# Kernel tuning notes

Hardware: AMD Instinct MI355X
Metric: run time of the kernel (lower is better)

## Reference

```python
import jax, jax.numpy as jnp
import numpy as np

N_NODES = 50000
N_EDGES = 1600000
NFEAT = 512
NHID = 64
H1 = 8      # nheads[0]
H2 = 1      # nheads[1]
NCLASS = 16
ALPHA = 0.2  # leaky_relu negative slope


def setup_inputs() -> dict:
    key = jax.random.key(0)
    ks = jax.random.split(key, 6)
    x = jax.random.normal(ks[0], (N_NODES, NFEAT), jnp.float32)
    edge_index = jax.random.randint(ks[1], (2, N_EDGES), 0, N_NODES, jnp.int32)

    def glorot(k, shape):
        fan_in, fan_out = shape[-2], shape[-1]
        std = (2.0 / (fan_in + fan_out)) ** 0.5
        return jax.random.normal(k, shape, jnp.float32) * std

    W1 = glorot(ks[2], (H1, NFEAT, NHID))
    a1 = jax.random.normal(ks[3], (H1, 2 * NHID), jnp.float32) * 0.1
    W2 = glorot(ks[4], (H2, NHID * H1, NCLASS))
    a2 = jax.random.normal(ks[5], (H2, 2 * NCLASS), jnp.float32) * 0.1
    return {"x": x, "edge_index": edge_index, "W1": W1, "a1": a1, "W2": W2, "a2": a2}


def _spgat_head(x, W, a, src, dst, n_nodes, apply_elu):
    # Sparse GAT head (pyGAT SpGraphAttentionLayer, eval mode / no dropout).
    h = x @ W                              # [N, F']
    f = W.shape[1]
    # a . [h_src || h_dst] decomposed into per-node scores (same math, no [E,2F'] concat)
    s_src = h @ a[:f]                      # [N]
    s_dst = h @ a[f:]                      # [N]
    logits = s_src[src] + s_dst[dst]       # [E]
    e = jnp.exp(-jax.nn.leaky_relu(logits, ALPHA))  # edge_e = exp(-leakyrelu(...)) > 0
    rowsum = jax.ops.segment_sum(e, src, num_segments=n_nodes)            # [N]
    agg = jax.ops.segment_sum(e[:, None] * h[dst], src, num_segments=n_nodes)  # [N, F']
    h_prime = agg / rowsum[:, None]
    return jax.nn.elu(h_prime) if apply_elu else h_prime


def reference(x, edge_index, W1, a1, W2, a2):
    src, dst = edge_index[0], edge_index[1]
    n = x.shape[0]
    # Layer 1: H1 heads, concat=True (elu inside each head), concatenated on features
    h = jnp.concatenate(
        [_spgat_head(x, W1[i], a1[i], src, dst, n, True) for i in range(W1.shape[0])],
        axis=1,
    )  # [N, H1*NHID]
    # Layer 2: H2 heads, concat=False, stacked then averaged
    outs = jnp.stack(
        [_spgat_head(h, W2[i], a2[i], src, dst, n, False) for i in range(W2.shape[0])],
        axis=2,
    )  # [N, NCLASS, H2]
    out = jnp.mean(outs, axis=2)
    return jax.nn.log_softmax(jax.nn.elu(out), axis=1)
```

## Files before the change

### kernel.cpp

```cpp
#include <hip/hip_runtime.h>

#define NN 50000
#define NE 1600000
#define NFEAT 512
#define NHID 64
#define H1 8
#define NCLASS 16
#define ALPHA 0.2f

#define BUCKETS 391
#define CAP 6144
#define EPB 4096
#define PASSA_BLKS 391
#define PASSB_BLKS 391
#define PACK_BLKS 1024
#define PACK2_BLKS 32
#define X8_BLKS 6250
#define GEMMB 391
#define NROW_PAD 50048

typedef __attribute__((ext_vector_type(8))) short short8;
typedef __attribute__((ext_vector_type(4))) float floatx4;
typedef __attribute__((ext_vector_type(2))) float floatx2;
typedef __attribute__((ext_vector_type(2))) long longx2;

__device__ __forceinline__ float elu_f(float x) { return x > 0.0f ? x : expf(x) - 1.0f; }
__device__ __forceinline__ float edge_w(float logit) {
    return expf(-fmaxf(logit, ALPHA * logit));
}
__device__ __forceinline__ ushort f2bf(float f) {
    uint u = __float_as_uint(f);
    return (ushort)((u + 0x7FFFu + ((u >> 16) & 1)) >> 16);
}
__device__ __forceinline__ uint packbf2(float lo, float hi) {
    return (uint)f2bf(lo) | ((uint)f2bf(hi) << 16);
}
__device__ __forceinline__ float bf2f(ushort v) { return __uint_as_float((uint)v << 16); }
__device__ __forceinline__ unsigned char f2fp8(float v) {
    return (unsigned char)(__builtin_amdgcn_cvt_pk_fp8_f32(v, v, 0, false) & 0xFF);
}
__device__ __forceinline__ uint pack4fp8(float a, float b, float c, float d) {
    uint u = __builtin_amdgcn_cvt_pk_fp8_f32(a, b, 0, false);
    return __builtin_amdgcn_cvt_pk_fp8_f32(c, d, u, true);
}

#define GLD16(g, l)                                                              \
    __builtin_amdgcn_global_load_lds(                                            \
        (const __attribute__((address_space(1))) unsigned int*)(g),              \
        (__attribute__((address_space(3))) unsigned int*)(l), 16, 0, 0)

__device__ __forceinline__ int scan256x(int v, int tid, int* wsum, int* tot) {
    int s = v;
#pragma unroll
    for (int o = 1; o < 64; o <<= 1) {
        int u = __shfl_up(s, o);
        if ((tid & 63) >= o) s += u;
    }
    __syncthreads();
    if ((tid & 63) == 63) wsum[tid >> 6] = s;
    __syncthreads();
    int off = 0, t = 0;
#pragma unroll
    for (int i = 0; i < 4; i++) {
        int x = wsum[i];
        if (i < (tid >> 6)) off += x;
        t += x;
    }
    *tot = t;
    return s - v + off;
}

__device__ __forceinline__ int scan512x(int v, int tid, int* wsum, int* tot) {
    int s = v;
#pragma unroll
    for (int o = 1; o < 64; o <<= 1) {
        int u = __shfl_up(s, o);
        if ((tid & 63) >= o) s += u;
    }
    __syncthreads();
    if ((tid & 63) == 63) wsum[tid >> 6] = s;
    __syncthreads();
    int off = 0, t = 0;
#pragma unroll
    for (int i = 0; i < 8; i++) {
        int x = wsum[i];
        if (i < (tid >> 6)) off += x;
        t += x;
    }
    *tot = t;
    return s - v + off;
}

__global__ __launch_bounds__(256) void prep_k(const float* __restrict__ W1,
                                              unsigned char* __restrict__ Wt8,
                                              const float* __restrict__ W2,
                                              ushort* __restrict__ W2tb,
                                              const float* __restrict__ x,
                                              unsigned char* x8,
                                              const int* __restrict__ ei,
                                              int* __restrict__ bucket_cnt,
                                              uint* __restrict__ staging) {
    int b = blockIdx.x;
    if (b < PACK_BLKS) {
        int i = b * 256 + threadIdx.x;
        int c = i >> 9, o = i & 511;
        int c6 = o >> 6, qhi = (o >> 4) & 3, kb = (o >> 3) & 1, bb = o & 7;
        int quad = qhi ^ ((c >> 1) & 3);
        int k = c6 * 64 + kb * 32 + quad * 8 + bb;
        Wt8[i] = f2fp8(W1[((c >> 6) * 512 + k) * 64 + (c & 63)]);
        return;
    }
    if (b < PACK_BLKS + PACK2_BLKS) {
        int i = (b - PACK_BLKS) * 256 + threadIdx.x;
        int c = i >> 9, f = i & 511;
        W2tb[i] = f2bf(W2[f * 16 + c]);
        return;
    }
    if (b < PACK_BLKS + PACK2_BLKS + X8_BLKS) {
        int i = (b - PACK_BLKS - PACK2_BLKS) * 256 + threadIdx.x;
        int row = i >> 5;
        int o0 = (i & 31) * 16;
        int c6 = o0 >> 6;
        int qhi = (o0 >> 4) & 3;
        int quad = qhi ^ ((row >> 1) & 3);
        const float* xp = x + (size_t)row * 512 + c6 * 64 + quad * 8;
        float4 v0 = *(const float4*)xp;
        float4 v1 = *(const float4*)(xp + 4);
        float4 v2 = *(const float4*)(xp + 32);
        float4 v3 = *(const float4*)(xp + 36);
        uint4 ov;
        ov.x = pack4fp8(v0.x, v0.y, v0.z, v0.w);
        ov.y = pack4fp8(v1.x, v1.y, v1.z, v1.w);
        ov.z = pack4fp8(v2.x, v2.y, v2.z, v2.w);
        ov.w = pack4fp8(v3.x, v3.y, v3.z, v3.w);
        *(uint4*)(x8 + (size_t)row * 512 + o0) = ov;
        return;
    }
    __shared__ int histA[BUCKETS];
    __shared__ int exclA[BUCKETS];
    __shared__ int baseA[BUCKETS];
    __shared__ int wsumA[4];
    __shared__ uint ebuf[EPB];
    const int blk = b - PACK_BLKS - PACK2_BLKS - X8_BLKS;
    const int t = threadIdx.x;
    const int e0 = blk * EPB;
    const int cntb = min(EPB, NE - e0);
    for (int i = t; i < BUCKETS; i += 256) histA[i] = 0;
    __syncthreads();
    int br[16]; uint pay[16];
#pragma unroll
    for (int i = 0; i < 16; i++) {
        int e = e0 + i * 256 + t;
        br[i] = -1;
        if (e < NE) {
            int s = ei[e], d = ei[NE + e];
            int bu = s >> 7;
            pay[i] = ((uint)bu << 23) | ((uint)(s & 127) << 16) | (uint)d;
            br[i] = (bu << 12) | atomicAdd(&histA[bu], 1);
        }
    }
    __syncthreads();
    int tot0, tot1;
    int v0 = histA[t];
    int v1 = (t + 256 < BUCKETS) ? histA[t + 256] : 0;
    int p0 = scan256x(v0, t, wsumA, &tot0);
    int p1 = scan256x(v1, t, wsumA, &tot1);
    exclA[t] = p0;
    if (t + 256 < BUCKETS) exclA[t + 256] = p1 + tot0;
    __syncthreads();
    for (int i = t; i < BUCKETS; i += 256) {
        int c = histA[i];
        if (c > 0) baseA[i] = atomicAdd(&bucket_cnt[i], c);
    }
#pragma unroll
    for (int i = 0; i < 16; i++)
        if (br[i] >= 0) ebuf[exclA[br[i] >> 12] + (br[i] & 4095)] = pay[i];
    __syncthreads();
    for (int j = t; j < cntb; j += 256) {
        uint v = ebuf[j];
        int bu = v >> 23;
        int pos = baseA[bu] + (j - exclA[bu]);
        staging[(size_t)bu * CAP + pos] = v;
    }
}

__global__ __launch_bounds__(64) void scan_k(const int* __restrict__ bucket_cnt,
                                             int* __restrict__ bucket_start,
                                             int* __restrict__ rowptr) {
    const int lane = threadIdx.x;
    int c[7]; int s0 = 0;
#pragma unroll
    for (int i = 0; i < 7; i++) {
        int b = lane * 7 + i;
        c[i] = (b < BUCKETS) ? bucket_cnt[b] : 0;
        s0 += c[i];
    }
    int sc = s0;
#pragma unroll
    for (int o = 1; o < 64; o <<= 1) {
        int u = __shfl_up(sc, o);
        if (lane >= o) sc += u;
    }
    int run = sc - s0;
#pragma unroll
    for (int i = 0; i < 7; i++) {
        int b = lane * 7 + i;
        if (b < BUCKETS) bucket_start[b] = run;
        run += c[i];
    }
    if (lane == 63) { bucket_start[BUCKETS] = run; rowptr[NN] = run; }
}

__global__ __launch_bounds__(512) void passb_gemm1_k(const int* __restrict__ bucket_cnt,
                                                     const int* __restrict__ bucket_start,
                                                     const uint* __restrict__ staging,
                                                     ushort* __restrict__ csru,
                                                     int* __restrict__ rowptr,
                                                     const unsigned char* __restrict__ Wt8,
                                                     const float* __restrict__ a1,
                                                     unsigned char* h8x8,
                                                     float* __restrict__ s1s,
                                                     float* __restrict__ s1d) {
    __shared__ unsigned char shmem[40960];
    const int tid = threadIdx.x;

    if (blockIdx.x < PASSB_BLKS) {
        int* hist2 = (int*)shmem;
        int* excl2 = hist2 + 128;
        int* cur2 = excl2 + 128;
        int* wsum2 = cur2 + 128;
        const int b = blockIdx.x;
        const int cnt = bucket_cnt[b];
        const int sbase = bucket_start[b];
        const uint* sg = staging + (size_t)b * CAP;
        if (tid < 128) { hist2[tid] = 0; cur2[tid] = 0; }
        __syncthreads();
        for (int e = tid; e < cnt; e += 512) atomicAdd(&hist2[(sg[e] >> 16) & 127], 1);
        __syncthreads();
        int v = (tid < 128) ? hist2[tid] : 0;
        int tot;
        int ex = scan512x(v, tid, wsum2, &tot);
        if (tid < 128) {
            excl2[tid] = ex;
            int n = b * 128 + tid;
            if (n < NN) rowptr[n] = sbase + ex;
        }
        __syncthreads();
        for (int e = tid; e < cnt; e += 512) {
            uint u = sg[e];
            int sl = (u >> 16) & 127;
            int pos = excl2[sl] + atomicAdd(&cur2[sl], 1);
            csru[sbase + pos] = (ushort)(u & 0xFFFF);
        }
        return;
    }

    unsigned char* As = shmem;
    unsigned char* Bs = shmem + 8192;
    const int gb = blockIdx.x - PASSB_BLKS;
    const int row0 = gb * 128;
    const int wv = tid >> 6, lane = tid & 63;
    const int l16 = lane & 15, quad = lane >> 4;
    const int qoff = ((quad ^ ((l16 >> 1) & 3)) << 4);
    const int mA = wv * 16 + (lane >> 2);
    const int offA = (lane & 3) * 16;
    const unsigned char* gA = h8x8 + (size_t)(row0 + mA) * 512 + offA;
    const unsigned char* gB0 = Wt8 + (size_t)(0 * 128 + mA) * 512 + offA;
    const unsigned char* gB1 = Wt8 + (size_t)(1 * 128 + mA) * 512 + offA;
    const unsigned char* gB2 = Wt8 + (size_t)(2 * 128 + mA) * 512 + offA;
    const unsigned char* gB3 = Wt8 + (size_t)(3 * 128 + mA) * 512 + offA;

    floatx4 acc[32];
#pragma unroll
    for (int ct = 0; ct < 32; ct++) acc[ct] = (floatx4){0.f, 0.f, 0.f, 0.f};

    for (int k0 = 0; k0 < 512; k0 += 64) {
        GLD16(gA + k0, As + wv * 1024);
        GLD16(gB0 + k0, Bs + wv * 1024);
        GLD16(gB1 + k0, Bs + 8192 + wv * 1024);
        GLD16(gB2 + k0, Bs + 16384 + wv * 1024);
        GLD16(gB3 + k0, Bs + 24576 + wv * 1024);
        __syncthreads();
        longx2 av = *(const longx2*)(As + (wv * 16 + l16) * 64 + qoff);
        const unsigned char* bp = Bs + l16 * 64 + qoff;
#pragma unroll
        for (int ct = 0; ct < 32; ct++) {
            longx2 bv = *(const longx2*)(bp + ct * 1024);
            acc[ct] = __builtin_amdgcn_mfma_f32_16x16x32_fp8_fp8(av.x, bv.x, acc[ct], 0, 0, 0);
            acc[ct] = __builtin_amdgcn_mfma_f32_16x16x32_fp8_fp8(av.y, bv.y, acc[ct], 0, 0, 0);
        }
        __syncthreads();
    }

    const int rbase = row0 + wv * 16 + quad * 4;
#pragma unroll
    for (int hh = 0; hh < 8; hh++) {
        float ss[4] = {0.f, 0.f, 0.f, 0.f}, sd[4] = {0.f, 0.f, 0.f, 0.f};
#pragma unroll
        for (int c4 = 0; c4 < 4; c4++) {
            int ct = hh * 4 + c4;
            int colg = ct * 16 + l16;
            float avs = a1[hh * 128 + c4 * 16 + l16];
            float avd = a1[hh * 128 + 64 + c4 * 16 + l16];
#pragma unroll
            for (int r = 0; r < 4; r++) {
                float v = acc[ct][r];
                ss[r] += v * avs;
                sd[r] += v * avd;
                int row = rbase + r;
                if (row < NN) h8x8[(size_t)row * 512 + colg] = f2fp8(v);
            }
        }
#pragma unroll
        for (int r = 0; r < 4; r++) {
            float a_ = ss[r], b_ = sd[r];
#pragma unroll
            for (int o = 1; o < 16; o <<= 1) {
                a_ += __shfl_xor(a_, o);
                b_ += __shfl_xor(b_, o);
            }
            int row = rbase + r;
            if (l16 == 0 && row < NN) {
                s1s[row * 8 + hh] = a_;
                s1d[row * 8 + hh] = b_;
            }
        }
    }
}

__global__ __launch_bounds__(256) void agg1f_k(const int* __restrict__ rowptr,
                                               const ushort* __restrict__ csru,
                                               const float* __restrict__ s1s,
                                               const float* __restrict__ s1d,
                                               const uint2* __restrict__ hb8,
                                               const ushort* __restrict__ W2tb,
                                               const float* __restrict__ a2,
                                               ushort* __restrict__ h2b,
                                               float* __restrict__ s2s,
                                               float* __restrict__ s2d) {
    __shared__ ushort Ash[16 * 512];
    const int tid = threadIdx.x;
    const int wv = tid >> 6, lane = tid & 63;
    const int n0 = blockIdx.x * 4;
    const int n = n0 + wv;
    const int head8 = lane >> 3;
    const int esub = lane & 7;
    const int beg = rowptr[n];
    const int deg = rowptr[n + 1] - beg;
    const float ssrc = s1s[n * 8 + head8];
    floatx2 acc[4] = {};
    float rsum = 0.f;

    int k = 0;
    for (; k + 8 <= deg; k += 8) {
        int dA = csru[beg + k + esub];
        float wA = edge_w(ssrc + s1d[dA * 8 + head8]);
        rsum += wA;
        int dj[8];
#pragma unroll
        for (int j = 0; j < 8; j++) dj[j] = __shfl(dA, j);
        uint2 v[8];
#pragma unroll
        for (int j = 0; j < 8; j++) v[j] = hb8[(uint)dj[j] * 64 + lane];
#pragma unroll
        for (int j = 0; j < 8; j++) {
            float wj = __shfl(wA, (head8 << 3) + j);
            floatx2 w2 = (floatx2){wj, wj};
            acc[0] += w2 * __builtin_amdgcn_cvt_pk_f32_fp8(v[j].x, false);
            acc[1] += w2 * __builtin_amdgcn_cvt_pk_f32_fp8(v[j].x, true);
            acc[2] += w2 * __builtin_amdgcn_cvt_pk_f32_fp8(v[j].y, false);
            acc[3] += w2 * __builtin_amdgcn_cvt_pk_f32_fp8(v[j].y, true);
        }
    }
    if (k < deg) {
        int jc = min(k + esub, deg - 1);
        int dwj = csru[beg + jc];
        float w = edge_w(ssrc + s1d[dwj * 8 + head8]);
        if (k + esub >= deg) w = 0.f;
        rsum += w;
        int rem = deg - k;
        for (int j = 0; j < rem; j++) {
            int djs = __shfl(dwj, j);
            uint2 vv = hb8[(uint)djs * 64 + lane];
            float wj = __shfl(w, (head8 << 3) + j);
            floatx2 w2 = (floatx2){wj, wj};
            acc[0] += w2 * __builtin_amdgcn_cvt_pk_f32_fp8(vv.x, false);
            acc[1] += w2 * __builtin_amdgcn_cvt_pk_f32_fp8(vv.x, true);
            acc[2] += w2 * __builtin_amdgcn_cvt_pk_f32_fp8(vv.y, false);
            acc[3] += w2 * __builtin_amdgcn_cvt_pk_f32_fp8(vv.y, true);
        }
    }

    rsum += __shfl_xor(rsum, 1);
    rsum += __shfl_xor(rsum, 2);
    rsum += __shfl_xor(rsum, 4);
    float inv = 1.0f / rsum;
    uint4 o;
    o.x = packbf2(elu_f(acc[0][0] * inv), elu_f(acc[0][1] * inv));
    o.y = packbf2(elu_f(acc[1][0] * inv), elu_f(acc[1][1] * inv));
    o.z = packbf2(elu_f(acc[2][0] * inv), elu_f(acc[2][1] * inv));
    o.w = packbf2(elu_f(acc[3][0] * inv), elu_f(acc[3][1] * inv));
    *(uint4*)(Ash + wv * 512 + lane * 8) = o;
    __syncthreads();

    if (wv == 0) {
        const int l16 = lane & 15, q = lane >> 4;
        floatx4 c2 = (floatx4){0.f, 0.f, 0.f, 0.f};
#pragma unroll
        for (int s = 0; s < 16; s++) {
            short8 af = *(const short8*)(Ash + l16 * 512 + s * 32 + q * 8);
            short8 bf = *(const short8*)(W2tb + l16 * 512 + s * 32 + q * 8);
            c2 = __builtin_amdgcn_mfma_f32_16x16x32_bf16(af, bf, c2, 0, 0, 0);
        }
        if (q == 0) {
#pragma unroll
            for (int r = 0; r < 4; r++) h2b[(size_t)(n0 + r) * 16 + l16] = f2bf(c2[r]);
        }
#pragma unroll
        for (int r = 0; r < 4; r++) {
            float ssv = c2[r] * a2[l16];
            float sdv = c2[r] * a2[16 + l16];
#pragma unroll
            for (int oo = 1; oo < 16; oo <<= 1) {
                ssv += __shfl_xor(ssv, oo);
                sdv += __shfl_xor(sdv, oo);
            }
            if (lane == 0) { s2s[n0 + r] = ssv; s2d[n0 + r] = sdv; }
        }
    }
}

__global__ __launch_bounds__(256) void agg2_k(const int* __restrict__ rowptr,
                                              const ushort* __restrict__ csru,
                                              const float* __restrict__ s2s,
                                              const float* __restrict__ s2d,
                                              const ushort* __restrict__ h2b,
                                              float* __restrict__ out) {
    const int n = (blockIdx.x * 256 + threadIdx.x) >> 6;
    const int lane = threadIdx.x & 63;
    if (n >= NN) return;
    const int beg = rowptr[n], end = rowptr[n + 1];
    const float sn = s2s[n];
    const int sub = lane >> 4, f = lane & 15;
    float acc = 0.f, rsum = 0.f;
    int e = beg + sub;
    for (; e + 12 < end; e += 16) {
        int d0 = csru[e], d1 = csru[e + 4], d2 = csru[e + 8], d3 = csru[e + 12];
        float t0 = s2d[d0], t1 = s2d[d1], t2 = s2d[d2], t3 = s2d[d3];
        float g0 = bf2f(h2b[(uint)d0 * 16 + f]), g1 = bf2f(h2b[(uint)d1 * 16 + f]);
        float g2 = bf2f(h2b[(uint)d2 * 16 + f]), g3 = bf2f(h2b[(uint)d3 * 16 + f]);
        float w0 = edge_w(sn + t0), w1 = edge_w(sn + t1);
        float w2 = edge_w(sn + t2), w3 = edge_w(sn + t3);
        acc += w0 * g0 + w1 * g1 + w2 * g2 + w3 * g3;
        rsum += w0 + w1 + w2 + w3;
    }
    for (; e < end; e += 4) {
        int d0 = csru[e];
        float w0 = edge_w(sn + s2d[d0]);
        acc += w0 * bf2f(h2b[(uint)d0 * 16 + f]);
        rsum += w0;
    }
    acc += __shfl_down(acc, 32);
    acc += __shfl_down(acc, 16);
    rsum += __shfl_down(rsum, 32);
    rsum += __shfl_down(rsum, 16);
    if (lane < 16) {
        float v = elu_f(acc / rsum);
        float m = v;
#pragma unroll
        for (int o = 8; o > 0; o >>= 1) m = fmaxf(m, __shfl_xor(m, o));
        float ex = expf(v - m), s = ex;
#pragma unroll
        for (int o = 8; o > 0; o >>= 1) s += __shfl_xor(s, o);
        out[(size_t)n * 16 + f] = v - (logf(s) + m);
    }
}

extern "C" void kernel_launch(void* const* d_in, const int* in_sizes, int n_in,
                              void* d_out, int out_size, void* d_ws, size_t ws_size,
                              hipStream_t stream) {
    const float* x  = (const float*)d_in[0];
    const int*   ei = (const int*)d_in[1];
    const float* W1 = (const float*)d_in[2];
    const float* a1 = (const float*)d_in[3];
    const float* W2 = (const float*)d_in[4];
    const float* a2 = (const float*)d_in[5];
    float* out = (float*)d_out;

    unsigned char* h8  = (unsigned char*)d_ws;
    unsigned char* Wt8 = h8 + (size_t)NROW_PAD * 512;
    ushort* W2tb  = (ushort*)(Wt8 + 512 * 512);
    float* s1s    = (float*)(W2tb + 8192);
    float* s1d    = s1s + (size_t)NN * H1;
    int* rowptr   = (int*)(s1d + (size_t)NN * H1);
    int* bucket_cnt   = rowptr + 50056;
    int* bucket_start = bucket_cnt + 512;
    ushort* csru  = (ushort*)(bucket_start + 512);
    ushort* h2b   = csru + NE;
    float* s2s    = (float*)(h2b + (size_t)NN * 16);
    float* s2d    = s2s + NN;
    uint* staging = (uint*)(s2d + NN);

    hipMemsetAsync(bucket_cnt, 0, 512 * sizeof(int), stream);

    prep_k<<<PACK_BLKS + PACK2_BLKS + X8_BLKS + PASSA_BLKS, 256, 0, stream>>>(
        W1, Wt8, W2, W2tb, x, h8, ei, bucket_cnt, staging);
    scan_k<<<1, 64, 0, stream>>>(bucket_cnt, bucket_start, rowptr);
    passb_gemm1_k<<<PASSB_BLKS + GEMMB, 512, 0, stream>>>(bucket_cnt, bucket_start,
                                                          staging, csru, rowptr,
                                                          Wt8, a1, h8, s1s, s1d);
    agg1f_k<<<NN / 4, 256, 0, stream>>>(rowptr, csru, s1s, s1d,
                                        (const uint2*)h8, W2tb, a2, h2b, s2s, s2d);
    agg2_k<<<(NN + 3) / 4, 256, 0, stream>>>(rowptr, csru, s2s, s2d, h2b, out);
}
```

Before: 401.4 us.

## Fold bucket scan into passB, prefetch edge scores, swizzle LDS, use fast exp

Removes the single-block scan kernel launch by having each passB block compute its own bucket offset with a wave-level prefix over the bucket counts. The layer-1 aggregation loop is restructured to merge the tail into the main loop and to prefetch the next group's neighbor indices and destination scores. The LDS staging buffer used by the MFMA is XOR-swizzled to reduce bank conflicts, and expf/logf calls become __expf/__logf. Each passB block now does the redundant scan work, and the fast intrinsics lower precision slightly.

```diff
diff --git a/kernel.cpp b/kernel.cpp
--- a/kernel.cpp
+++ b/kernel.cpp
@@ -24,9 +24,9 @@
 typedef __attribute__((ext_vector_type(2))) float floatx2;
 typedef __attribute__((ext_vector_type(2))) long longx2;
 
-__device__ __forceinline__ float elu_f(float x) { return x > 0.0f ? x : expf(x) - 1.0f; }
+__device__ __forceinline__ float elu_f(float x) { return x > 0.0f ? x : __expf(x) - 1.0f; }
 __device__ __forceinline__ float edge_w(float logit) {
-    return expf(-fmaxf(logit, ALPHA * logit));
+    return __expf(-fmaxf(logit, ALPHA * logit));
 }
 __device__ __forceinline__ ushort f2bf(float f) {
     uint u = __float_as_uint(f);
@@ -184,35 +184,7 @@
     }
 }
 
-__global__ __launch_bounds__(64) void scan_k(const int* __restrict__ bucket_cnt,
-                                             int* __restrict__ bucket_start,
-                                             int* __restrict__ rowptr) {
-    const int lane = threadIdx.x;
-    int c[7]; int s0 = 0;
-#pragma unroll
-    for (int i = 0; i < 7; i++) {
-        int b = lane * 7 + i;
-        c[i] = (b < BUCKETS) ? bucket_cnt[b] : 0;
-        s0 += c[i];
-    }
-    int sc = s0;
-#pragma unroll
-    for (int o = 1; o < 64; o <<= 1) {
-        int u = __shfl_up(sc, o);
-        if (lane >= o) sc += u;
-    }
-    int run = sc - s0;
-#pragma unroll
-    for (int i = 0; i < 7; i++) {
-        int b = lane * 7 + i;
-        if (b < BUCKETS) bucket_start[b] = run;
-        run += c[i];
-    }
-    if (lane == 63) { bucket_start[BUCKETS] = run; rowptr[NN] = run; }
-}
-
 __global__ __launch_bounds__(512) void passb_gemm1_k(const int* __restrict__ bucket_cnt,
-                                                     const int* __restrict__ bucket_start,
                                                      const uint* __restrict__ staging,
                                                      ushort* __restrict__ csru,
                                                      int* __restrict__ rowptr,
@@ -229,12 +201,35 @@
         int* excl2 = hist2 + 128;
         int* cur2 = excl2 + 128;
         int* wsum2 = cur2 + 128;
+        __shared__ int sbs;
         const int b = blockIdx.x;
         const int cnt = bucket_cnt[b];
-        const int sbase = bucket_start[b];
         const uint* sg = staging + (size_t)b * CAP;
         if (tid < 128) { hist2[tid] = 0; cur2[tid] = 0; }
+        if (tid < 64) {
+            int c[7]; int s0 = 0;
+#pragma unroll
+            for (int i = 0; i < 7; i++) {
+                int bi = tid * 7 + i;
+                c[i] = (bi < BUCKETS) ? bucket_cnt[bi] : 0;
+                s0 += c[i];
+            }
+            int sc = s0;
+#pragma unroll
+            for (int o = 1; o < 64; o <<= 1) {
+                int u = __shfl_up(sc, o);
+                if (tid >= o) sc += u;
+            }
+            int run = sc - s0;
+            if (tid == b / 7) {
+                int part = run;
+                for (int i = 0; i < b % 7; i++) part += c[i];
+                sbs = part;
+            }
+        }
+        if (b == 0 && tid == 0) rowptr[NN] = NE;
         __syncthreads();
+        const int sbase = sbs;
         for (int e = tid; e < cnt; e += 512) atomicAdd(&hist2[(sg[e] >> 16) & 127], 1);
         __syncthreads();
         int v = (tid < 128) ? hist2[tid] : 0;
@@ -339,11 +334,13 @@
                                                float* __restrict__ s2s,
                                                float* __restrict__ s2d) {
     __shared__ ushort Ash[16 * 512];
+    unsigned char* ashb = (unsigned char*)Ash;
     const int tid = threadIdx.x;
     const int wv = tid >> 6, lane = tid & 63;
     const int n0 = blockIdx.x * 4;
     const int n = n0 + wv;
     const int head8 = lane >> 3;
+    const int hb = head8 << 3;
     const int esub = lane & 7;
     const int beg = rowptr[n];
     const int deg = rowptr[n + 1] - beg;
@@ -351,43 +348,33 @@
     floatx2 acc[4] = {};
     float rsum = 0.f;
 
-    int k = 0;
-    for (; k + 8 <= deg; k += 8) {
-        int dA = csru[beg + k + esub];
-        float wA = edge_w(ssrc + s1d[dA * 8 + head8]);
-        rsum += wA;
-        int dj[8];
-#pragma unroll
-        for (int j = 0; j < 8; j++) dj[j] = __shfl(dA, j);
-        uint2 v[8];
-#pragma unroll
-        for (int j = 0; j < 8; j++) v[j] = hb8[(uint)dj[j] * 64 + lane];
-#pragma unroll
-        for (int j = 0; j < 8; j++) {
-            float wj = __shfl(wA, (head8 << 3) + j);
-            floatx2 w2 = (floatx2){wj, wj};
-            acc[0] += w2 * __builtin_amdgcn_cvt_pk_f32_fp8(v[j].x, false);
-            acc[1] += w2 * __builtin_amdgcn_cvt_pk_f32_fp8(v[j].x, true);
-            acc[2] += w2 * __builtin_amdgcn_cvt_pk_f32_fp8(v[j].y, false);
-            acc[3] += w2 * __builtin_amdgcn_cvt_pk_f32_fp8(v[j].y, true);
-        }
-    }
-    if (k < deg) {
-        int jc = min(k + esub, deg - 1);
-        int dwj = csru[beg + jc];
-        float w = edge_w(ssrc + s1d[dwj * 8 + head8]);
-        if (k + esub >= deg) w = 0.f;
-        rsum += w;
-        int rem = deg - k;
-        for (int j = 0; j < rem; j++) {
-            int djs = __shfl(dwj, j);
-            uint2 vv = hb8[(uint)djs * 64 + lane];
-            float wj = __shfl(w, (head8 << 3) + j);
-            floatx2 w2 = (floatx2){wj, wj};
-            acc[0] += w2 * __builtin_amdgcn_cvt_pk_f32_fp8(vv.x, false);
-            acc[1] += w2 * __builtin_amdgcn_cvt_pk_f32_fp8(vv.x, true);
-            acc[2] += w2 * __builtin_amdgcn_cvt_pk_f32_fp8(vv.y, false);
-            acc[3] += w2 * __builtin_amdgcn_cvt_pk_f32_fp8(vv.y, true);
+    const int G = (deg + 7) >> 3;
+    const int dm1 = deg - 1;
+    if (G > 0) {
+        int dA = csru[beg + min(esub, dm1)];
+        float tw = s1d[dA * 8 + head8];
+        for (int g = 0; g < G; g++) {
+            uint2 v[8];
+#pragma unroll
+            for (int j = 0; j < 8; j++) {
+                int dj = __shfl(dA, j);
+                v[j] = hb8[(uint)dj * 64 + lane];
+            }
+            int dAn = csru[beg + min(g * 8 + 8 + esub, dm1)];
+            float twn = s1d[dAn * 8 + head8];
+            float w = (g * 8 + esub <= dm1) ? edge_w(ssrc + tw) : 0.f;
+            rsum += w;
+#pragma unroll
+            for (int j = 0; j < 8; j++) {
+                float wj = __shfl(w, hb + j);
+                floatx2 w2 = (floatx2){wj, wj};
+                acc[0] += w2 * __builtin_amdgcn_cvt_pk_f32_fp8(v[j].x, false);
+                acc[1] += w2 * __builtin_amdgcn_cvt_pk_f32_fp8(v[j].x, true);
+                acc[2] += w2 * __builtin_amdgcn_cvt_pk_f32_fp8(v[j].y, false);
+                acc[3] += w2 * __builtin_amdgcn_cvt_pk_f32_fp8(v[j].y, true);
+            }
+            dA = dAn;
+            tw = twn;
         }
     }
 
@@ -400,7 +387,7 @@
     o.y = packbf2(elu_f(acc[1][0] * inv), elu_f(acc[1][1] * inv));
     o.z = packbf2(elu_f(acc[2][0] * inv), elu_f(acc[2][1] * inv));
     o.w = packbf2(elu_f(acc[3][0] * inv), elu_f(acc[3][1] * inv));
-    *(uint4*)(Ash + wv * 512 + lane * 8) = o;
+    *(uint4*)(ashb + wv * 1024 + ((lane * 16) ^ (wv << 4))) = o;
     __syncthreads();
 
     if (wv == 0) {
@@ -408,7 +395,8 @@
         floatx4 c2 = (floatx4){0.f, 0.f, 0.f, 0.f};
 #pragma unroll
         for (int s = 0; s < 16; s++) {
-            short8 af = *(const short8*)(Ash + l16 * 512 + s * 32 + q * 8);
+            short8 af = *(const short8*)(ashb + l16 * 1024 +
+                                         ((s * 64 + q * 16) ^ ((l16 & 7) << 4)));
             short8 bf = *(const short8*)(W2tb + l16 * 512 + s * 32 + q * 8);
             c2 = __builtin_amdgcn_mfma_f32_16x16x32_bf16(af, bf, c2, 0, 0, 0);
         }
@@ -469,10 +457,10 @@
         float m = v;
 #pragma unroll
         for (int o = 8; o > 0; o >>= 1) m = fmaxf(m, __shfl_xor(m, o));
-        float ex = expf(v - m), s = ex;
+        float ex = __expf(v - m), s = ex;
 #pragma unroll
         for (int o = 8; o > 0; o >>= 1) s += __shfl_xor(s, o);
-        out[(size_t)n * 16 + f] = v - (logf(s) + m);
+        out[(size_t)n * 16 + f] = v - (__logf(s) + m);
     }
 }
 
@@ -505,9 +493,7 @@
 
     prep_k<<<PACK_BLKS + PACK2_BLKS + X8_BLKS + PASSA_BLKS, 256, 0, stream>>>(
         W1, Wt8, W2, W2tb, x, h8, ei, bucket_cnt, staging);
-    scan_k<<<1, 64, 0, stream>>>(bucket_cnt, bucket_start, rowptr);
-    passb_gemm1_k<<<PASSB_BLKS + GEMMB, 512, 0, stream>>>(bucket_cnt, bucket_start,
-                                                          staging, csru, rowptr,
+    passb_gemm1_k<<<PASSB_BLKS + GEMMB, 512, 0, stream>>>(bucket_cnt, staging, csru, rowptr,
                                                           Wt8, a1, h8, s1s, s1d);
     agg1f_k<<<NN / 4, 256, 0, stream>>>(rowptr, csru, s1s, s1d,
                                         (const uint2*)h8, W2tb, a2, h2b, s2s, s2d);
```

Measured after the change: 396.7 us. No clear change (-1.2%).
